# Kernel optimization log

Hardware: AMD Instinct MI355X
Metric: run time of the kernel (lower is better)

The kernel has to match this reference:

```python
import jax, jax.numpy as jnp
import numpy as np

EPS = 1e-7  # Keras K.epsilon()


def setup_inputs() -> dict:
    key = jax.random.key(0)
    ks = jax.random.split(key, 8)
    B, T, D = 64, 2048, 256
    context = jax.random.normal(ks[0], (B, T, D), dtype=jnp.float32)
    aspect = jax.random.normal(ks[1], (B, D), dtype=jnp.float32)
    sentence = jax.random.normal(ks[2], (B, D), dtype=jnp.float32)
    context_mask = jax.random.randint(ks[3], (B, T), 0, 2).astype(bool)
    context_w = jax.random.normal(ks[4], (D, D), dtype=jnp.float32) * 0.05
    aspect_w = jax.random.normal(ks[5], (D, D), dtype=jnp.float32) * 0.05
    sent_w = jax.random.normal(ks[6], (D, D), dtype=jnp.float32) * 0.05
    attend_w = jax.random.normal(ks[7], (D, 1), dtype=jnp.float32) * 0.05
    return {"context": context, "aspect": aspect, "sentence": sentence,
            "context_mask": context_mask, "context_w": context_w,
            "aspect_w": aspect_w, "sent_w": sent_w, "attend_w": attend_w}


def reference(context, aspect, sentence, context_mask, context_w, aspect_w, sent_w, attend_w):
    # bias term from aspect/sentence, broadcast over time instead of K.repeat: [B,1,D]
    bias = (aspect @ aspect_w + sentence @ sent_w)[:, None, :]
    h = jnp.tanh(jnp.einsum('btd,de->bte', context, context_w) + bias)  # [B,T,D]
    g = jnp.einsum('btd,d->bt', h, attend_w[:, 0])                      # [B,T]
    a = jnp.exp(g) * context_mask.astype(jnp.float32)                   # faithful: no max-subtract
    a = a / (jnp.sum(a, axis=-1, keepdims=True) + EPS)
    attend_context = jnp.einsum('btd,bt->bd', context, a) + sentence     # [B,D]
    return attend_context
```

## Files before the change

### kernel.cpp

```cpp
#include <hip/hip_runtime.h>
#include <hip/hip_bf16.h>

#define BB  64
#define TT  2048
#define DD  256
#define EPSV 1e-7f
#define TILE_R 32
#define NTILE  8
#define NBLK   512
#define PITCH  528
#define TILEB  16896

#define TANH_PRE 2.8853900817779268f
#define LOG2E    1.4426950408889634f

typedef __attribute__((ext_vector_type(8))) short bf16x8;
typedef __attribute__((ext_vector_type(4))) float f32x4;

__device__ __forceinline__ ushort f2bf(float f) {
    union { float f; unsigned u; } v; v.f = f;
    unsigned u = v.u;
    unsigned r = (u + 0x7FFFu + ((u >> 16) & 1u)) >> 16;
    return (ushort)r;
}

__device__ __forceinline__ float bf2f(unsigned h16) {
    union { unsigned u; float f; } v; v.u = h16 << 16;
    return v.f;
}

__device__ __forceinline__ unsigned pkbf(float lo, float hi) {
    union { float f; unsigned u; } a, b;
    a.f = lo; b.f = hi;
    return __builtin_amdgcn_perm(b.u + 0x8000u, a.u + 0x8000u, 0x07060302u);
}

__device__ __forceinline__ float tanh_pre(float y) {
    float e = __builtin_amdgcn_exp2f(y);
    return fmaf(-2.0f, __builtin_amdgcn_rcpf(e + 1.0f), 1.0f);
}

template<int CTRL>
__device__ __forceinline__ float dpp_rot_add(float x) {
    union { float f; int i; } a; a.f = x;
    int r = __builtin_amdgcn_update_dpp(0, a.i, CTRL, 0xF, 0xF, true);
    union { int i; float f; } b; b.i = r;
    return x + b.f;
}
__device__ __forceinline__ float row16_sum(float x) {
    x = dpp_rot_add<0x121>(x);
    x = dpp_rot_add<0x122>(x);
    x = dpp_rot_add<0x124>(x);
    x = dpp_rot_add<0x128>(x);
    return x;
}

__global__ __launch_bounds__(256) void prep_kernel(
    const float* __restrict__ aspect, const float* __restrict__ sentence,
    const float* __restrict__ context_w, const float* __restrict__ aspect_w,
    const float* __restrict__ sent_w,
    float* __restrict__ bias_part, ushort* __restrict__ wfrag_ws)
{
    const int blk = blockIdx.x, tid = threadIdx.x;
    if (blk < 512) {
        const int b = blk >> 3, q = blk & 7, e = tid;
        float s = 0.f;
        #pragma unroll 4
        for (int dd = 0; dd < 32; ++dd) {
            const int d = q * 32 + dd;
            s = fmaf(aspect[b * DD + d],   aspect_w[d * DD + e], s);
            s = fmaf(sentence[b * DD + d], sent_w[d * DD + e],   s);
        }
        bias_part[blk * DD + e] = s;
    } else {
        const int flat = (blk - 512) * 256 + tid;
        const int lane = flat & 63;
        const int kn   = flat >> 6;
        const int kk   = kn >> 4;
        const int n    = kn & 15;
        const int krow = kk * 32 + ((lane >> 4) << 3);
        const int col  = n * 16 + (lane & 15);
        bf16x8 v;
        #pragma unroll
        for (int j = 0; j < 8; ++j)
            v[j] = (short)f2bf(context_w[(size_t)(krow + j) * DD + col] * TANH_PRE);
        *reinterpret_cast<bf16x8*>(wfrag_ws + (size_t)flat * 8) = v;
    }
}

__global__ __launch_bounds__(512, 2) void attn_main(
    const float* __restrict__ ctx, const int* __restrict__ mask,
    const float* __restrict__ attend_w,
    const float* __restrict__ bias_part, const ushort* __restrict__ wfrag_ws,
    float* __restrict__ partial_ws, float* __restrict__ esum_ws)
{
    __shared__ __align__(16) char bfb[4][TILEB];
    __shared__ float gpartT[2][8][TILE_R];
    __shared__ float bias_lds[256];
    __shared__ float aw_lds[256];
    __shared__ float mask_lds[256];

    const int tid  = threadIdx.x;
    const int wave = tid >> 6;
    const int lane = tid & 63;
    const int blk  = blockIdx.x;
    const int b    = blk >> 3;
    const int cg   = wave;
    const int l15  = lane & 15, hi = lane >> 4;

    if (tid < 256) {
        float bs = 0.f;
        #pragma unroll
        for (int q = 0; q < 8; ++q) bs += bias_part[(b * 8 + q) * DD + tid];
        bias_lds[tid] = bs * TANH_PRE;
    } else {
        const int m = tid - 256;
        aw_lds[m]   = attend_w[m] * LOG2E;
        mask_lds[m] = (float)mask[blk * 256 + m];
    }

    bf16x8 Bf[8][2];
    {
        const bf16x8* wf = reinterpret_cast<const bf16x8*>(wfrag_ws);
        #pragma unroll
        for (int kk = 0; kk < 8; ++kk) {
            Bf[kk][0] = wf[(kk * 16 + cg * 2 + 0) * 64 + lane];
            Bf[kk][1] = wf[(kk * 16 + cg * 2 + 1) * 64 + lane];
        }
    }

    const float4* src = reinterpret_cast<const float4*>(ctx);
    const int crow0 = tid >> 5,          c80 = tid & 31;
    const int crow1 = (512 + tid) >> 5,  c81 = (512 + tid) & 31;
    const int coff0 = crow0 * PITCH + c80 * 16;
    const int coff1 = crow1 * PITCH + c81 * 16;
    const int abase = l15 * PITCH + hi * 16;
    const int wbase = wave * 4 * PITCH + lane * 8;

    float4 sreg[4];
    {
        const size_t base4 = (size_t)(blk * NTILE) * 2048;
        #pragma unroll
        for (int i = 0; i < 2; ++i) {
            const int c = i * 512 + tid;
            sreg[2 * i + 0] = src[base4 + 2 * c + 0];
            sreg[2 * i + 1] = src[base4 + 2 * c + 1];
        }
        char* dst = bfb[0];
        #pragma unroll
        for (int i = 0; i < 2; ++i) {
            uint4 u;
            u.x = pkbf(sreg[2 * i].x,     sreg[2 * i].y);
            u.y = pkbf(sreg[2 * i].z,     sreg[2 * i].w);
            u.z = pkbf(sreg[2 * i + 1].x, sreg[2 * i + 1].y);
            u.w = pkbf(sreg[2 * i + 1].z, sreg[2 * i + 1].w);
            *reinterpret_cast<uint4*>(dst + (i ? coff1 : coff0)) = u;
        }
        const size_t b1 = (size_t)(blk * NTILE + 1) * 2048;
        #pragma unroll
        for (int i = 0; i < 2; ++i) {
            const int c = i * 512 + tid;
            sreg[2 * i + 0] = src[b1 + 2 * c + 0];
            sreg[2 * i + 1] = src[b1 + 2 * c + 1];
        }
    }
    __syncthreads();

    const int c0 = cg * 32 + l15, c1 = c0 + 16;
    const float bs0 = bias_lds[c0], awc0 = aw_lds[c0];
    const float bs1 = bias_lds[c1], awc1 = aw_lds[c1];

    float accd[4] = {0.f, 0.f, 0.f, 0.f};
    float es_acc = 0.f;

    auto do_wsum = [&](int t) {
        const char* pb = bfb[t & 3] + wbase;
        const int gp = t & 1;
        const int erow = lane & 31;
        float gsum = 0.f;
        #pragma unroll
        for (int c = 0; c < 8; ++c) gsum += gpartT[gp][c][erow];
        const float ev = __builtin_amdgcn_exp2f(gsum) * mask_lds[t * TILE_R + erow];
        es_acc += (lane < 32) ? ev : 0.f;
        #pragma unroll
        for (int rr = 0; rr < 4; ++rr) {
            const int r = wave * 4 + rr;
            const float e = __shfl(ev, r);
            const uint2 hv = *reinterpret_cast<const uint2*>(pb + rr * PITCH);
            accd[0] = fmaf(bf2f(hv.x & 0xffffu), e, accd[0]);
            accd[1] = fmaf(bf2f(hv.x >> 16),     e, accd[1]);
            accd[2] = fmaf(bf2f(hv.y & 0xffffu), e, accd[2]);
            accd[3] = fmaf(bf2f(hv.y >> 16),     e, accd[3]);
        }
    };

    for (int it = 0; it < NTILE; ++it) {
        const char* lb = bfb[it & 3];

        if (it > 0) do_wsum(it - 1);

        if (it + 1 < NTILE) {
            char* dst = bfb[(it + 1) & 3];
            #pragma unroll
            for (int i = 0; i < 2; ++i) {
                uint4 u;
                u.x = pkbf(sreg[2 * i].x,     sreg[2 * i].y);
                u.y = pkbf(sreg[2 * i].z,     sreg[2 * i].w);
                u.z = pkbf(sreg[2 * i + 1].x, sreg[2 * i + 1].y);
                u.w = pkbf(sreg[2 * i + 1].z, sreg[2 * i + 1].w);
                *reinterpret_cast<uint4*>(dst + (i ? coff1 : coff0)) = u;
            }
        }
        if (it + 2 < NTILE) {
            const size_t base4 = (size_t)(blk * NTILE + it + 2) * 2048;
            #pragma unroll
            for (int i = 0; i < 2; ++i) {
                const int c = i * 512 + tid;
                sreg[2 * i + 0] = src[base4 + 2 * c + 0];
                sreg[2 * i + 1] = src[base4 + 2 * c + 1];
            }
        }

        f32x4 acc[2][2];
        #pragma unroll
        for (int rt = 0; rt < 2; ++rt) {
            acc[rt][0] = (f32x4){0.f, 0.f, 0.f, 0.f};
            acc[rt][1] = (f32x4){0.f, 0.f, 0.f, 0.f};
        }
        {
            const char* ab = lb + abase;
            #pragma unroll
            for (int rt = 0; rt < 2; ++rt) {
                #pragma unroll
                for (int kk = 0; kk < 8; ++kk) {
                    const bf16x8 a = *reinterpret_cast<const bf16x8*>(
                        ab + rt * 16 * PITCH + kk * 64);
                    acc[rt][0] = __builtin_amdgcn_mfma_f32_16x16x32_bf16(a, Bf[kk][0], acc[rt][0], 0, 0, 0);
                    acc[rt][1] = __builtin_amdgcn_mfma_f32_16x16x32_bf16(a, Bf[kk][1], acc[rt][1], 0, 0, 0);
                }
            }
        }

        const int gp = it & 1;
        #pragma unroll
        for (int rt = 0; rt < 2; ++rt) {
            float g0 = row16_sum(tanh_pre(acc[rt][0][0] + bs0) * awc0
                               + tanh_pre(acc[rt][1][0] + bs1) * awc1);
            float g1 = row16_sum(tanh_pre(acc[rt][0][1] + bs0) * awc0
                               + tanh_pre(acc[rt][1][1] + bs1) * awc1);
            float g2 = row16_sum(tanh_pre(acc[rt][0][2] + bs0) * awc0
                               + tanh_pre(acc[rt][1][2] + bs1) * awc1);
            float g3 = row16_sum(tanh_pre(acc[rt][0][3] + bs0) * awc0
                               + tanh_pre(acc[rt][1][3] + bs1) * awc1);
            if (l15 == 0) {
                const int r = rt * 16 + (hi << 2);
                *reinterpret_cast<float4*>(&gpartT[gp][cg][r]) = (float4){g0, g1, g2, g3};
            }
        }
        __syncthreads();
    }

    do_wsum(NTILE - 1);

    {
        float* part_d = reinterpret_cast<float*>(bfb[0]);
        *reinterpret_cast<float4*>(&part_d[wave * 256 + lane * 4]) =
            (float4){accd[0], accd[1], accd[2], accd[3]};
    }
    __syncthreads();
    if (tid < 256) {
        const float* part_d = reinterpret_cast<const float*>(bfb[0]);
        float s = 0.f;
        #pragma unroll
        for (int w = 0; w < 8; ++w) s += part_d[w * 256 + tid];
        partial_ws[blk * DD + tid] = s;
    }
    if (wave == 0) {
        float s = row16_sum(es_acc);
        s += __shfl_xor(s, 16);
        if (lane == 0) esum_ws[blk] = s;
    }
}

__global__ __launch_bounds__(256) void finalize_kernel(
    const float* __restrict__ sentence, const float* __restrict__ partial_ws,
    const float* __restrict__ esum_ws, float* __restrict__ out)
{
    const int b = blockIdx.x, d = threadIdx.x;
    float es = 0.f, s = 0.f;
    #pragma unroll
    for (int i = 0; i < 8; ++i) {
        es += esum_ws[b * 8 + i];
        s  += partial_ws[(size_t)(b * 8 + i) * DD + d];
    }
    out[b * DD + d] = s / (es + EPSV) + sentence[b * DD + d];
}

extern "C" void kernel_launch(void* const* d_in, const int* in_sizes, int n_in,
                              void* d_out, int out_size, void* d_ws, size_t ws_size,
                              hipStream_t stream)
{
    const float* ctx       = (const float*)d_in[0];
    const float* aspect    = (const float*)d_in[1];
    const float* sentence  = (const float*)d_in[2];
    const int*   mask      = (const int*)  d_in[3];
    const float* context_w = (const float*)d_in[4];
    const float* aspect_w  = (const float*)d_in[5];
    const float* sent_w    = (const float*)d_in[6];
    const float* attend_w  = (const float*)d_in[7];
    float* out = (float*)d_out;

    char* ws = (char*)d_ws;
    ushort* wfrag_ws   = (ushort*)(ws);
    float*  bias_part  = (float*) (ws + 131072);
    float*  esum_ws    = (float*) (ws + 131072 + 524288);
    float*  partial_ws = (float*) (ws + 131072 + 524288 + 2048);

    prep_kernel<<<544, 256, 0, stream>>>(aspect, sentence, context_w, aspect_w, sent_w,
                                         bias_part, wfrag_ws);
    attn_main<<<NBLK, 512, 0, stream>>>(ctx, mask, attend_w, bias_part, wfrag_ws,
                                        partial_ws, esum_ws);
    finalize_kernel<<<BB, 256, 0, stream>>>(sentence, partial_ws, esum_ws, out);
}
```

Baseline: 45.05 us.

## Split MFMA work across waves by row half and four column tiles

Changes the per-wave MFMA tiling from 1 column group × 2 row tiles to 2 row halves × 4 column tiles. Each wave now loads one A fragment per k-step and reuses it across four B fragments, halving LDS A-reads and the cross-wave partial reduction (4 groups instead of 8). The cost is twice as many resident B-fragment registers (64 bf16x8 VGPR groups), which may increase register pressure under launch_bounds(512,2).

```diff
diff --git a/kernel.cpp b/kernel.cpp
--- a/kernel.cpp
+++ b/kernel.cpp
@@ -95,7 +95,7 @@
     float* __restrict__ partial_ws, float* __restrict__ esum_ws)
 {
     __shared__ __align__(16) char bfb[4][TILEB];
-    __shared__ float gpartT[2][8][TILE_R];
+    __shared__ float gpartT[2][4][TILE_R];
     __shared__ float bias_lds[256];
     __shared__ float aw_lds[256];
     __shared__ float mask_lds[256];
@@ -105,7 +105,8 @@
     const int lane = tid & 63;
     const int blk  = blockIdx.x;
     const int b    = blk >> 3;
-    const int cg   = wave;
+    const int rh   = wave >> 2;
+    const int cg   = wave & 3;
     const int l15  = lane & 15, hi = lane >> 4;
 
     if (tid < 256) {
@@ -119,13 +120,14 @@
         mask_lds[m] = (float)mask[blk * 256 + m];
     }
 
-    bf16x8 Bf[8][2];
+    bf16x8 Bf[8][4];
     {
         const bf16x8* wf = reinterpret_cast<const bf16x8*>(wfrag_ws);
         #pragma unroll
         for (int kk = 0; kk < 8; ++kk) {
-            Bf[kk][0] = wf[(kk * 16 + cg * 2 + 0) * 64 + lane];
-            Bf[kk][1] = wf[(kk * 16 + cg * 2 + 1) * 64 + lane];
+            #pragma unroll
+            for (int n = 0; n < 4; ++n)
+                Bf[kk][n] = wf[(kk * 16 + cg * 4 + n) * 64 + lane];
         }
     }
 
@@ -134,7 +136,7 @@
     const int crow1 = (512 + tid) >> 5,  c81 = (512 + tid) & 31;
     const int coff0 = crow0 * PITCH + c80 * 16;
     const int coff1 = crow1 * PITCH + c81 * 16;
-    const int abase = l15 * PITCH + hi * 16;
+    const int abase = (rh * 16 + l15) * PITCH + hi * 16;
     const int wbase = wave * 4 * PITCH + lane * 8;
 
     float4 sreg[4];
@@ -166,9 +168,13 @@
     }
     __syncthreads();
 
-    const int c0 = cg * 32 + l15, c1 = c0 + 16;
-    const float bs0 = bias_lds[c0], awc0 = aw_lds[c0];
-    const float bs1 = bias_lds[c1], awc1 = aw_lds[c1];
+    float bsn[4], awn[4];
+    #pragma unroll
+    for (int n = 0; n < 4; ++n) {
+        const int c = (cg * 4 + n) * 16 + l15;
+        bsn[n] = bias_lds[c];
+        awn[n] = aw_lds[c];
+    }
 
     float accd[4] = {0.f, 0.f, 0.f, 0.f};
     float es_acc = 0.f;
@@ -179,7 +185,7 @@
         const int erow = lane & 31;
         float gsum = 0.f;
         #pragma unroll
-        for (int c = 0; c < 8; ++c) gsum += gpartT[gp][c][erow];
+        for (int c = 0; c < 4; ++c) gsum += gpartT[gp][c][erow];
         const float ev = __builtin_amdgcn_exp2f(gsum) * mask_lds[t * TILE_R + erow];
         es_acc += (lane < 32) ? ev : 0.f;
         #pragma unroll
@@ -221,40 +227,35 @@
             }
         }
 
-        f32x4 acc[2][2];
-        #pragma unroll
-        for (int rt = 0; rt < 2; ++rt) {
-            acc[rt][0] = (f32x4){0.f, 0.f, 0.f, 0.f};
-            acc[rt][1] = (f32x4){0.f, 0.f, 0.f, 0.f};
-        }
+        f32x4 acc[4];
+        #pragma unroll
+        for (int n = 0; n < 4; ++n) acc[n] = (f32x4){0.f, 0.f, 0.f, 0.f};
         {
             const char* ab = lb + abase;
             #pragma unroll
-            for (int rt = 0; rt < 2; ++rt) {
+            for (int kk = 0; kk < 8; ++kk) {
+                const bf16x8 a = *reinterpret_cast<const bf16x8*>(ab + kk * 64);
                 #pragma unroll
-                for (int kk = 0; kk < 8; ++kk) {
-                    const bf16x8 a = *reinterpret_cast<const bf16x8*>(
-                        ab + rt * 16 * PITCH + kk * 64);
-                    acc[rt][0] = __builtin_amdgcn_mfma_f32_16x16x32_bf16(a, Bf[kk][0], acc[rt][0], 0, 0, 0);
-                    acc[rt][1] = __builtin_amdgcn_mfma_f32_16x16x32_bf16(a, Bf[kk][1], acc[rt][1], 0, 0, 0);
-                }
+                for (int n = 0; n < 4; ++n)
+                    acc[n] = __builtin_amdgcn_mfma_f32_16x16x32_bf16(a, Bf[kk][n], acc[n], 0, 0, 0);
             }
         }
 
         const int gp = it & 1;
-        #pragma unroll
-        for (int rt = 0; rt < 2; ++rt) {
-            float g0 = row16_sum(tanh_pre(acc[rt][0][0] + bs0) * awc0
-                               + tanh_pre(acc[rt][1][0] + bs1) * awc1);
-            float g1 = row16_sum(tanh_pre(acc[rt][0][1] + bs0) * awc0
-                               + tanh_pre(acc[rt][1][1] + bs1) * awc1);
-            float g2 = row16_sum(tanh_pre(acc[rt][0][2] + bs0) * awc0
-                               + tanh_pre(acc[rt][1][2] + bs1) * awc1);
-            float g3 = row16_sum(tanh_pre(acc[rt][0][3] + bs0) * awc0
-                               + tanh_pre(acc[rt][1][3] + bs1) * awc1);
+        {
+            float g[4];
+            #pragma unroll
+            for (int j = 0; j < 4; ++j) {
+                float gv = tanh_pre(acc[0][j] + bsn[0]) * awn[0]
+                         + tanh_pre(acc[1][j] + bsn[1]) * awn[1]
+                         + tanh_pre(acc[2][j] + bsn[2]) * awn[2]
+                         + tanh_pre(acc[3][j] + bsn[3]) * awn[3];
+                g[j] = row16_sum(gv);
+            }
             if (l15 == 0) {
-                const int r = rt * 16 + (hi << 2);
-                *reinterpret_cast<float4*>(&gpartT[gp][cg][r]) = (float4){g0, g1, g2, g3};
+                const int r = rh * 16 + (hi << 2);
+                *reinterpret_cast<float4*>(&gpartT[gp][cg][r]) =
+                    (float4){g[0], g[1], g[2], g[3]};
             }
         }
         __syncthreads();
```

New measurement: 42.25 us, median of 2. 6.2% less time.
